# Optimization experiments

Hardware: AMD Instinct MI355X
Metric: run time of the kernel (lower is better)

## Reference

```python
import jax, jax.numpy as jnp
import numpy as np

N_NODES = 100000
N_EDGES = 1600000
N_GRAPHS = 256
F_NODE, F_EDGE, HID, OUT = 64, 16, 128, 128
BN_SCALE = 1.0 / np.sqrt(1.0 + 1e-5)  # BatchNorm eval with running mean 0, var 1


def setup_inputs() -> dict:
    key = jax.random.key(0)
    ks = iter(jax.random.split(key, 64))
    inp = {}
    inp["x"] = jax.random.normal(next(ks), (N_NODES, F_NODE), dtype=jnp.float32)
    inp["edge_attr"] = jax.random.normal(next(ks), (N_EDGES, F_EDGE), dtype=jnp.float32)
    inp["edge_index"] = jax.random.randint(next(ks), (2, N_EDGES), 0, N_NODES)
    inp["batch"] = jnp.sort(jax.random.randint(next(ks), (N_NODES,), 0, N_GRAPHS))

    def p(shape, scale):
        return (jax.random.normal(next(ks), shape, dtype=jnp.float32) * scale)

    in_dims = [F_NODE, HID, HID]
    for i, d in enumerate(in_dims):
        inp[f"el_w{i}"] = p((F_EDGE, d), F_EDGE ** -0.5)
        inp[f"el_b{i}"] = jnp.zeros((d,), jnp.float32)
        inp[f"c{i}_w1"] = p((d, HID), d ** -0.5)
        inp[f"c{i}_b1"] = jnp.zeros((HID,), jnp.float32)
        inp[f"c{i}_g"] = jnp.ones((HID,), jnp.float32)
        inp[f"c{i}_bt"] = jnp.zeros((HID,), jnp.float32)
        inp[f"c{i}_w2"] = p((HID, HID), HID ** -0.5)
        inp[f"c{i}_b2"] = jnp.zeros((HID,), jnp.float32)
    inp["o_w1"] = p((HID, OUT), HID ** -0.5)
    inp["o_b1"] = jnp.zeros((OUT,), jnp.float32)
    inp["o_w2"] = p((OUT, OUT), OUT ** -0.5)
    inp["o_b2"] = jnp.zeros((OUT,), jnp.float32)
    return inp


def reference(x, edge_attr,
              el_w0, el_b0, c0_w1, c0_b1, c0_g, c0_bt, c0_w2, c0_b2,
              el_w1, el_b1, c1_w1, c1_b1, c1_g, c1_bt, c1_w2, c1_b2,
              el_w2, el_b2, c2_w1, c2_b1, c2_g, c2_bt, c2_w2, c2_b2,
              o_w1, o_b1, o_w2, o_b2,
              edge_index, batch):
    src, dst = edge_index[0], edge_index[1]
    n = x.shape[0]
    layers = [
        (el_w0, el_b0, c0_w1, c0_b1, c0_g, c0_bt, c0_w2, c0_b2),
        (el_w1, el_b1, c1_w1, c1_b1, c1_g, c1_bt, c1_w2, c1_b2),
        (el_w2, el_b2, c2_w1, c2_b1, c2_g, c2_bt, c2_w2, c2_b2),
    ]
    h = x
    for (ew, eb, w1, b1, g, bt, w2, b2) in layers:
        ea = edge_attr @ ew + eb                              # [E, d]
        msg = jax.nn.relu(h[src] + ea)                        # GINEConv message
        agg = jax.ops.segment_sum(msg, dst, num_segments=n)   # scatter-sum to targets
        hh = h + agg                                          # (1+eps)*x + aggr, eps=0
        hh = hh @ w1 + b1                                     # MLP: Linear
        hh = g * (hh * BN_SCALE) + bt                         # BatchNorm1d (eval)
        hh = jax.nn.relu(hh)
        hh = hh @ w2 + b2                                     # MLP: Linear
        h = jax.nn.relu(hh)                                   # dropout(p=0, eval) + act
    s = jax.ops.segment_sum(h, batch, num_segments=N_GRAPHS)
    cnt = jax.ops.segment_sum(jnp.ones((n,), h.dtype), batch, num_segments=N_GRAPHS)
    pooled = s / jnp.maximum(cnt, 1.0)[:, None]               # scatter-mean pooling
    out = jax.nn.relu(pooled @ o_w1 + o_b1) @ o_w2 + o_b2     # out_lin
    return out
```

## Files before the change

kernel.cpp:

```cpp
#include <hip/hip_runtime.h>
#include <hip/hip_fp16.h>
#include <cstdint>
#include <cstddef>

#define N_NODES_C  100000
#define N_EDGES_C  1600000
#define N_GRAPHS_C 256
#define HID_C      128
#define BN_SCALE_C 0.9999950000374997f

#define SCAN_B 1024
#define SCAN_NB ((N_NODES_C + SCAN_B - 1) / SCAN_B)

struct __align__(16) H8 { __half2 v[4]; };

__global__ __launch_bounds__(256) void hist_kernel(
    const int* __restrict__ dst, int* __restrict__ counts, int n_edges)
{
    int e = blockIdx.x * 256 + threadIdx.x;
    if (e < n_edges) atomicAdd(&counts[dst[e]], 1);
}

__global__ __launch_bounds__(SCAN_B) void scan1_kernel(
    const int* __restrict__ counts, int* __restrict__ incl,
    int* __restrict__ blocksums, int n)
{
    __shared__ int sdata[SCAN_B];
    const int lid = threadIdx.x;
    const int i = blockIdx.x * SCAN_B + lid;
    sdata[lid] = (i < n) ? counts[i] : 0;
    __syncthreads();
#pragma unroll
    for (int off = 1; off < SCAN_B; off <<= 1) {
        int t = (lid >= off) ? sdata[lid - off] : 0;
        __syncthreads();
        sdata[lid] += t;
        __syncthreads();
    }
    if (i < n) incl[i] = sdata[lid];
    if (lid == SCAN_B - 1) blocksums[blockIdx.x] = sdata[lid];
}

__global__ void scan2_kernel(const int* __restrict__ blocksums,
                             int* __restrict__ blockoffs, int nb)
{
    if (threadIdx.x == 0 && blockIdx.x == 0) {
        int off = 0;
        for (int b = 0; b < nb; ++b) { blockoffs[b] = off; off += blocksums[b]; }
    }
}

__global__ __launch_bounds__(SCAN_B) void scan3_kernel(
    int* __restrict__ incl, const int* __restrict__ blockoffs, int n)
{
    const int i = blockIdx.x * SCAN_B + threadIdx.x;
    if (i < n) incl[i] += blockoffs[blockIdx.x];
}

__global__ __launch_bounds__(256) void initrows_kernel(
    const int* __restrict__ incl, const int* __restrict__ counts,
    int* __restrict__ rowstart, int* __restrict__ cursor, int n)
{
    const int i = blockIdx.x * 256 + threadIdx.x;
    if (i < n) {
        const int rs = incl[i] - counts[i];
        rowstart[i] = rs;
        cursor[i]   = rs;
    }
}

__global__ __launch_bounds__(256) void scatter_kernel(
    const int* __restrict__ src, const int* __restrict__ dst,
    int* __restrict__ cursor, int* __restrict__ perm_src,
    int* __restrict__ perm_eid, int n_edges)
{
    const int e = blockIdx.x * 256 + threadIdx.x;
    if (e < n_edges) {
        const int pos = atomicAdd(&cursor[dst[e]], 1);
        perm_src[pos] = src[e];
        perm_eid[pos] = e;
    }
}

__global__ __launch_bounds__(256) void permute_ea_f16_kernel(
    const float* __restrict__ edge_attr, const int* __restrict__ perm_eid,
    __half* __restrict__ ea_f16, int n_edges)
{
    const int j = blockIdx.x * 256 + threadIdx.x;
    if (j >= n_edges) return;
    const int eid = perm_eid[j];
    const float4* p = (const float4*)(edge_attr + (size_t)eid * 16);
    const float4 q0 = p[0], q1 = p[1], q2 = p[2], q3 = p[3];
    H8 a, b;
    a.v[0] = __floats2half2_rn(q0.x, q0.y);
    a.v[1] = __floats2half2_rn(q0.z, q0.w);
    a.v[2] = __floats2half2_rn(q1.x, q1.y);
    a.v[3] = __floats2half2_rn(q1.z, q1.w);
    b.v[0] = __floats2half2_rn(q2.x, q2.y);
    b.v[1] = __floats2half2_rn(q2.z, q2.w);
    b.v[2] = __floats2half2_rn(q3.x, q3.y);
    b.v[3] = __floats2half2_rn(q3.z, q3.w);
    H8* o = (H8*)(ea_f16 + (size_t)j * 16);
    o[0] = a;
    o[1] = b;
}

__device__ __forceinline__ float4 eamlp_f16(const H8* __restrict__ p,
                                            const __half2 (*ew2)[4],
                                            const float4 ebv)
{
    const H8 a = p[0], b = p[1];
    __half2 c0 = {0.f, 0.f}, c1 = {0.f, 0.f}, c2 = {0.f, 0.f}, c3 = {0.f, 0.f};
#pragma unroll
    for (int k2 = 0; k2 < 4; ++k2) {
        c0 = __hfma2(a.v[k2], ew2[k2][0], c0);
        c1 = __hfma2(a.v[k2], ew2[k2][1], c1);
        c2 = __hfma2(a.v[k2], ew2[k2][2], c2);
        c3 = __hfma2(a.v[k2], ew2[k2][3], c3);
    }
#pragma unroll
    for (int k2 = 0; k2 < 4; ++k2) {
        c0 = __hfma2(b.v[k2], ew2[4 + k2][0], c0);
        c1 = __hfma2(b.v[k2], ew2[4 + k2][1], c1);
        c2 = __hfma2(b.v[k2], ew2[4 + k2][2], c2);
        c3 = __hfma2(b.v[k2], ew2[4 + k2][3], c3);
    }
    float4 m;
    m.x = ebv.x + __low2float(c0) + __high2float(c0);
    m.y = ebv.y + __low2float(c1) + __high2float(c1);
    m.z = ebv.z + __low2float(c2) + __high2float(c2);
    m.w = ebv.w + __low2float(c3) + __high2float(c3);
    return m;
}

template<int DIN>
__global__ __launch_bounds__(256) void gine_agg_kernel(
    const float* __restrict__ h, const __half* __restrict__ ea_f16,
    const int* __restrict__ perm_src,
    const int* __restrict__ rowstart, const int* __restrict__ rowend,
    const float* __restrict__ ew, const float* __restrict__ eb,
    float* __restrict__ agg, int n_nodes)
{
    constexpr int NQ    = DIN / 4;
    constexpr int SLOTS = 256 / NQ;
    const int fq   = threadIdx.x & (NQ - 1);
    const int slot = threadIdx.x / NQ;
    const int v = blockIdx.x * SLOTS + slot;
    if (v >= n_nodes) return;

    __half2 ew2[8][4];
#pragma unroll
    for (int k2 = 0; k2 < 8; ++k2)
#pragma unroll
        for (int fi = 0; fi < 4; ++fi)
            ew2[k2][fi] = __floats2half2_rn(ew[(size_t)(2 * k2)     * DIN + fq * 4 + fi],
                                            ew[(size_t)(2 * k2 + 1) * DIN + fq * 4 + fi]);
    const float4 ebv = *(const float4*)(eb + fq * 4);

    const int s0 = rowstart[v];
    const int s1 = rowend[v];

    float4 acc = {0.f, 0.f, 0.f, 0.f};
    int j = s0;
    for (; j + 2 <= s1; j += 2) {
        const int sn0 = perm_src[j + 0];
        const int sn1 = perm_src[j + 1];
        const float4 hv0 = *(const float4*)(h + (size_t)sn0 * DIN + fq * 4);
        const float4 hv1 = *(const float4*)(h + (size_t)sn1 * DIN + fq * 4);
        const H8* p0 = (const H8*)(ea_f16 + (size_t)(j + 0) * 16);
        const H8* p1 = (const H8*)(ea_f16 + (size_t)(j + 1) * 16);
        const float4 m0 = eamlp_f16(p0, ew2, ebv);
        const float4 m1 = eamlp_f16(p1, ew2, ebv);
        acc.x += fmaxf(m0.x + hv0.x, 0.f) + fmaxf(m1.x + hv1.x, 0.f);
        acc.y += fmaxf(m0.y + hv0.y, 0.f) + fmaxf(m1.y + hv1.y, 0.f);
        acc.z += fmaxf(m0.z + hv0.z, 0.f) + fmaxf(m1.z + hv1.z, 0.f);
        acc.w += fmaxf(m0.w + hv0.w, 0.f) + fmaxf(m1.w + hv1.w, 0.f);
    }
    if (j < s1) {
        const int sn = perm_src[j];
        const float4 hv = *(const float4*)(h + (size_t)sn * DIN + fq * 4);
        const H8* p = (const H8*)(ea_f16 + (size_t)j * 16);
        const float4 m = eamlp_f16(p, ew2, ebv);
        acc.x += fmaxf(m.x + hv.x, 0.f);
        acc.y += fmaxf(m.y + hv.y, 0.f);
        acc.z += fmaxf(m.z + hv.z, 0.f);
        acc.w += fmaxf(m.w + hv.w, 0.f);
    }
    *(float4*)(agg + (size_t)v * DIN + fq * 4) = acc;
}

#define OUT4(acc, a0, a1, a2, a3, wv)                                     \
    do {                                                                  \
        acc[0][0] = fmaf(a0, wv.x, acc[0][0]);                            \
        acc[0][1] = fmaf(a0, wv.y, acc[0][1]);                            \
        acc[0][2] = fmaf(a0, wv.z, acc[0][2]);                            \
        acc[0][3] = fmaf(a0, wv.w, acc[0][3]);                            \
        acc[1][0] = fmaf(a1, wv.x, acc[1][0]);                            \
        acc[1][1] = fmaf(a1, wv.y, acc[1][1]);                            \
        acc[1][2] = fmaf(a1, wv.z, acc[1][2]);                            \
        acc[1][3] = fmaf(a1, wv.w, acc[1][3]);                            \
        acc[2][0] = fmaf(a2, wv.x, acc[2][0]);                            \
        acc[2][1] = fmaf(a2, wv.y, acc[2][1]);                            \
        acc[2][2] = fmaf(a2, wv.z, acc[2][2]);                            \
        acc[2][3] = fmaf(a2, wv.w, acc[2][3]);                            \
        acc[3][0] = fmaf(a3, wv.x, acc[3][0]);                            \
        acc[3][1] = fmaf(a3, wv.y, acc[3][1]);                            \
        acc[3][2] = fmaf(a3, wv.z, acc[3][2]);                            \
        acc[3][3] = fmaf(a3, wv.w, acc[3][3]);                            \
    } while (0)

template<int DIN>
__global__ __launch_bounds__(256) void node_kernel(
    const float* __restrict__ h, const float* __restrict__ agg,
    const float* __restrict__ w1, const float* __restrict__ b1,
    const float* __restrict__ gm, const float* __restrict__ bt,
    const float* __restrict__ w2, const float* __restrict__ b2,
    float* __restrict__ hout, int n_nodes)
{
    constexpr int SX = DIN + 4;
    constexpr int ST = HID_C + 4;
    __shared__ float s_x[32][SX];
    __shared__ float s_t[32][ST];

    const int tid = threadIdx.x;
    const int fg = tid & 31;
    const int ng = tid >> 5;
    const int base = blockIdx.x * 32;

    constexpr int KQ = DIN / 4;
    for (int idx = tid; idx < 32 * KQ; idx += 256) {
        const int ni = idx / KQ;
        const int k4 = (idx - ni * KQ) * 4;
        const int node = base + ni;
        const float4 hv = *(const float4*)(h   + (size_t)node * DIN + k4);
        const float4 av = *(const float4*)(agg + (size_t)node * DIN + k4);
        float4 s; s.x = hv.x + av.x; s.y = hv.y + av.y;
        s.z = hv.z + av.z; s.w = hv.w + av.w;
        *(float4*)(&s_x[ni][k4]) = s;
    }
    __syncthreads();

    {
        const float4 b1v = *(const float4*)(b1 + fg * 4);
        float acc[4][4];
#pragma unroll
        for (int ni = 0; ni < 4; ++ni) {
            acc[ni][0] = b1v.x; acc[ni][1] = b1v.y;
            acc[ni][2] = b1v.z; acc[ni][3] = b1v.w;
        }
        for (int k = 0; k < DIN; k += 4) {
            const float4 x0 = *(const float4*)(&s_x[ng * 4 + 0][k]);
            const float4 x1 = *(const float4*)(&s_x[ng * 4 + 1][k]);
            const float4 x2 = *(const float4*)(&s_x[ng * 4 + 2][k]);
            const float4 x3 = *(const float4*)(&s_x[ng * 4 + 3][k]);
            const float4 wa = *(const float4*)(w1 + (size_t)(k + 0) * HID_C + fg * 4);
            const float4 wb = *(const float4*)(w1 + (size_t)(k + 1) * HID_C + fg * 4);
            const float4 wc = *(const float4*)(w1 + (size_t)(k + 2) * HID_C + fg * 4);
            const float4 wd = *(const float4*)(w1 + (size_t)(k + 3) * HID_C + fg * 4);
            OUT4(acc, x0.x, x1.x, x2.x, x3.x, wa);
            OUT4(acc, x0.y, x1.y, x2.y, x3.y, wb);
            OUT4(acc, x0.z, x1.z, x2.z, x3.z, wc);
            OUT4(acc, x0.w, x1.w, x2.w, x3.w, wd);
        }
        const float4 gv  = *(const float4*)(gm + fg * 4);
        const float4 btv = *(const float4*)(bt + fg * 4);
#pragma unroll
        for (int ni = 0; ni < 4; ++ni) {
            float4 tv;
            tv.x = fmaxf(fmaf(acc[ni][0] * BN_SCALE_C, gv.x, btv.x), 0.f);
            tv.y = fmaxf(fmaf(acc[ni][1] * BN_SCALE_C, gv.y, btv.y), 0.f);
            tv.z = fmaxf(fmaf(acc[ni][2] * BN_SCALE_C, gv.z, btv.z), 0.f);
            tv.w = fmaxf(fmaf(acc[ni][3] * BN_SCALE_C, gv.w, btv.w), 0.f);
            *(float4*)(&s_t[ng * 4 + ni][fg * 4]) = tv;
        }
    }
    __syncthreads();

    {
        const float4 b2v = *(const float4*)(b2 + fg * 4);
        float acc[4][4];
#pragma unroll
        for (int ni = 0; ni < 4; ++ni) {
            acc[ni][0] = b2v.x; acc[ni][1] = b2v.y;
            acc[ni][2] = b2v.z; acc[ni][3] = b2v.w;
        }
        for (int k = 0; k < HID_C; k += 4) {
            const float4 x0 = *(const float4*)(&s_t[ng * 4 + 0][k]);
            const float4 x1 = *(const float4*)(&s_t[ng * 4 + 1][k]);
            const float4 x2 = *(const float4*)(&s_t[ng * 4 + 2][k]);
            const float4 x3 = *(const float4*)(&s_t[ng * 4 + 3][k]);
            const float4 wa = *(const float4*)(w2 + (size_t)(k + 0) * HID_C + fg * 4);
            const float4 wb = *(const float4*)(w2 + (size_t)(k + 1) * HID_C + fg * 4);
            const float4 wc = *(const float4*)(w2 + (size_t)(k + 2) * HID_C + fg * 4);
            const float4 wd = *(const float4*)(w2 + (size_t)(k + 3) * HID_C + fg * 4);
            OUT4(acc, x0.x, x1.x, x2.x, x3.x, wa);
            OUT4(acc, x0.y, x1.y, x2.y, x3.y, wb);
            OUT4(acc, x0.z, x1.z, x2.z, x3.z, wc);
            OUT4(acc, x0.w, x1.w, x2.w, x3.w, wd);
        }
#pragma unroll
        for (int ni = 0; ni < 4; ++ni) {
            const int node = base + ng * 4 + ni;
            float4 ov;
            ov.x = fmaxf(acc[ni][0], 0.f);
            ov.y = fmaxf(acc[ni][1], 0.f);
            ov.z = fmaxf(acc[ni][2], 0.f);
            ov.w = fmaxf(acc[ni][3], 0.f);
            *(float4*)(hout + (size_t)node * HID_C + fg * 4) = ov;
        }
    }
}

__global__ __launch_bounds__(256) void pool_kernel(
    const float* __restrict__ hfin, const int* __restrict__ batch,
    const float* __restrict__ w1, const float* __restrict__ b1,
    const float* __restrict__ w2, const float* __restrict__ b2,
    float* __restrict__ out, int n_nodes)
{
    const int gid = blockIdx.x;

    int lo = 0, hi = n_nodes;
    while (lo < hi) { int mid = (lo + hi) >> 1; if (batch[mid] < gid) lo = mid + 1; else hi = mid; }
    const int start = lo;
    hi = n_nodes;
    while (lo < hi) { int mid = (lo + hi) >> 1; if (batch[mid] < gid + 1) lo = mid + 1; else hi = mid; }
    const int end = lo;

    const int f = threadIdx.x & (HID_C - 1);
    const int half = threadIdx.x >> 7;

    float sum = 0.f;
    for (int n = start + half; n < end; n += 2)
        sum += hfin[(size_t)n * HID_C + f];

    __shared__ float s_sum[2][HID_C];
    __shared__ float s_p[HID_C];
    __shared__ float s_t[HID_C];
    s_sum[half][f] = sum;
    __syncthreads();

    if (threadIdx.x < HID_C) {
        const float cnt = (float)(end - start);
        s_p[f] = (s_sum[0][f] + s_sum[1][f]) / fmaxf(cnt, 1.f);
    }
    __syncthreads();

    if (threadIdx.x < HID_C) {
        float acc = b1[f];
        for (int k = 0; k < HID_C; ++k) acc = fmaf(s_p[k], w1[k * HID_C + f], acc);
        s_t[f] = fmaxf(acc, 0.f);
    }
    __syncthreads();

    if (threadIdx.x < HID_C) {
        float acc = b2[f];
        for (int k = 0; k < HID_C; ++k) acc = fmaf(s_t[k], w2[k * HID_C + f], acc);
        out[(size_t)gid * HID_C + f] = acc;
    }
}

extern "C" void kernel_launch(void* const* d_in, const int* in_sizes, int n_in,
                              void* d_out, int out_size, void* d_ws, size_t ws_size,
                              hipStream_t stream)
{
    const float* x         = (const float*)d_in[0];
    const float* edge_attr = (const float*)d_in[1];
    const int*   edge_index= (const int*)  d_in[2];
    const int*   batch     = (const int*)  d_in[3];
    const int*   src = edge_index;
    const int*   dst = edge_index + N_EDGES_C;

    const float* el_w[3] = {(const float*)d_in[4],  (const float*)d_in[12], (const float*)d_in[20]};
    const float* el_b[3] = {(const float*)d_in[5],  (const float*)d_in[13], (const float*)d_in[21]};
    const float* c_w1[3] = {(const float*)d_in[6],  (const float*)d_in[14], (const float*)d_in[22]};
    const float* c_b1[3] = {(const float*)d_in[7],  (const float*)d_in[15], (const float*)d_in[23]};
    const float* c_g [3] = {(const float*)d_in[8],  (const float*)d_in[16], (const float*)d_in[24]};
    const float* c_bt[3] = {(const float*)d_in[9],  (const float*)d_in[17], (const float*)d_in[25]};
    const float* c_w2[3] = {(const float*)d_in[10], (const float*)d_in[18], (const float*)d_in[26]};
    const float* c_b2[3] = {(const float*)d_in[11], (const float*)d_in[19], (const float*)d_in[27]};
    const float* o_w1 = (const float*)d_in[28];
    const float* o_b1 = (const float*)d_in[29];
    const float* o_w2 = (const float*)d_in[30];
    const float* o_b2 = (const float*)d_in[31];

    char* wsp = (char*)d_ws;
    size_t used = 0;
    auto alloc = [&](size_t bytes) { char* p = wsp + used; used += (bytes + 255) & ~(size_t)255; return p; };
    float* h        = (float*)alloc((size_t)N_NODES_C * HID_C * 4);
    float* agg      = (float*)alloc((size_t)N_NODES_C * HID_C * 4);
    int*   counts   = (int*)alloc((size_t)N_NODES_C * 4);
    int*   incl     = (int*)alloc((size_t)N_NODES_C * 4);
    int*   rowstart = (int*)alloc((size_t)N_NODES_C * 4);
    int*   cursor   = (int*)alloc((size_t)N_NODES_C * 4);
    int*   blocksums= (int*)alloc(128 * 4);
    int*   blockoffs= (int*)alloc(128 * 4);
    int*   perm_src = (int*)alloc((size_t)N_EDGES_C * 4);
    int*   perm_eid = (int*)alloc((size_t)N_EDGES_C * 4);
    __half* ea_f16  = (__half*)alloc((size_t)N_EDGES_C * 16 * 2);
    (void)ws_size;

    hipMemsetAsync(counts, 0, (size_t)N_NODES_C * 4, stream);
    hist_kernel<<<(N_EDGES_C + 255) / 256, 256, 0, stream>>>(dst, counts, N_EDGES_C);
    scan1_kernel<<<SCAN_NB, SCAN_B, 0, stream>>>(counts, incl, blocksums, N_NODES_C);
    scan2_kernel<<<1, 64, 0, stream>>>(blocksums, blockoffs, SCAN_NB);
    scan3_kernel<<<SCAN_NB, SCAN_B, 0, stream>>>(incl, blockoffs, N_NODES_C);
    initrows_kernel<<<(N_NODES_C + 255) / 256, 256, 0, stream>>>(incl, counts, rowstart,
                                                                 cursor, N_NODES_C);
    scatter_kernel<<<(N_EDGES_C + 255) / 256, 256, 0, stream>>>(src, dst, cursor,
                                                                perm_src, perm_eid, N_EDGES_C);
    permute_ea_f16_kernel<<<(N_EDGES_C + 255) / 256, 256, 0, stream>>>(
        edge_attr, perm_eid, ea_f16, N_EDGES_C);

    for (int l = 0; l < 3; ++l) {
        const float* hin = (l == 0) ? x : h;
        if (l == 0) {
            gine_agg_kernel<64><<<(N_NODES_C + 15) / 16, 256, 0, stream>>>(
                hin, ea_f16, perm_src, rowstart, incl, el_w[0], el_b[0],
                agg, N_NODES_C);
            node_kernel<64><<<N_NODES_C / 32, 256, 0, stream>>>(
                hin, agg, c_w1[0], c_b1[0], c_g[0], c_bt[0], c_w2[0], c_b2[0],
                h, N_NODES_C);
        } else {
            gine_agg_kernel<128><<<(N_NODES_C + 7) / 8, 256, 0, stream>>>(
                hin, ea_f16, perm_src, rowstart, incl, el_w[l], el_b[l],
                agg, N_NODES_C);
            node_kernel<128><<<N_NODES_C / 32, 256, 0, stream>>>(
                hin, agg, c_w1[l], c_b1[l], c_g[l], c_bt[l], c_w2[l], c_b2[l],
                h, N_NODES_C);
        }
    }

    pool_kernel<<<N_GRAPHS_C, 256, 0, stream>>>(h, batch, o_w1, o_b1, o_w2, o_b2,
                                                (float*)d_out, N_NODES_C);
}
```

Measured before the change: 1.163 ms.

## Gather fp16 node features in aggregation and run node MLP on MFMA

The edge aggregation now gathers source-node features from an fp16 copy of h (and of x for layer 0), which halves the bytes moved by the random gather. The node MLP is rewritten as a per-wave 16-node tile using mfma_f32_16x16x32_f16, with the weights pre-transposed to fp16 by small setup kernels. The node kernel also emits the fp16 copy of h for the next layer. The cost is extra fp16 rounding of activations and weights, plus a few setup kernels and extra writes.

```diff
diff --git a/kernel.cpp b/kernel.cpp
--- a/kernel.cpp
+++ b/kernel.cpp
@@ -12,7 +12,12 @@
 #define SCAN_B 1024
 #define SCAN_NB ((N_NODES_C + SCAN_B - 1) / SCAN_B)
 
+typedef _Float16 h8 __attribute__((ext_vector_type(8)));
+typedef _Float16 h4 __attribute__((ext_vector_type(4)));
+typedef float    f4 __attribute__((ext_vector_type(4)));
+
 struct __align__(16) H8 { __half2 v[4]; };
+struct __align__(8)  Hq { __half2 a, b; };
 
 __global__ __launch_bounds__(256) void hist_kernel(
     const int* __restrict__ dst, int* __restrict__ counts, int n_edges)
@@ -105,6 +110,27 @@
     o[1] = b;
 }
 
+__global__ __launch_bounds__(256) void cast_f16_kernel(
+    const float* __restrict__ in, _Float16* __restrict__ out, int n4)
+{
+    const int i = blockIdx.x * 256 + threadIdx.x;
+    if (i >= n4) return;
+    const float4 v = ((const float4*)in)[i];
+    h4 o; o[0] = (_Float16)v.x; o[1] = (_Float16)v.y;
+    o[2] = (_Float16)v.z; o[3] = (_Float16)v.w;
+    *(h4*)(out + (size_t)i * 4) = o;
+}
+
+__global__ __launch_bounds__(256) void transpose_w_kernel(
+    const float* __restrict__ w, _Float16* __restrict__ wt, int K, int N)
+{
+    const int i = blockIdx.x * 256 + threadIdx.x;
+    if (i >= K * N) return;
+    const int n = i / K;
+    const int k = i - n * K;
+    wt[(size_t)n * K + k] = (_Float16)w[(size_t)k * N + n];
+}
+
 __device__ __forceinline__ float4 eamlp_f16(const H8* __restrict__ p,
                                             const __half2 (*ew2)[4],
                                             const float4 ebv)
@@ -135,7 +161,7 @@
 
 template<int DIN>
 __global__ __launch_bounds__(256) void gine_agg_kernel(
-    const float* __restrict__ h, const __half* __restrict__ ea_f16,
+    const __half* __restrict__ h16, const __half* __restrict__ ea_f16,
     const int* __restrict__ perm_src,
     const int* __restrict__ rowstart, const int* __restrict__ rowend,
     const float* __restrict__ ew, const float* __restrict__ eb,
@@ -165,148 +191,107 @@
     for (; j + 2 <= s1; j += 2) {
         const int sn0 = perm_src[j + 0];
         const int sn1 = perm_src[j + 1];
-        const float4 hv0 = *(const float4*)(h + (size_t)sn0 * DIN + fq * 4);
-        const float4 hv1 = *(const float4*)(h + (size_t)sn1 * DIN + fq * 4);
+        const Hq hq0 = *(const Hq*)(h16 + (size_t)sn0 * DIN + fq * 4);
+        const Hq hq1 = *(const Hq*)(h16 + (size_t)sn1 * DIN + fq * 4);
         const H8* p0 = (const H8*)(ea_f16 + (size_t)(j + 0) * 16);
         const H8* p1 = (const H8*)(ea_f16 + (size_t)(j + 1) * 16);
         const float4 m0 = eamlp_f16(p0, ew2, ebv);
         const float4 m1 = eamlp_f16(p1, ew2, ebv);
-        acc.x += fmaxf(m0.x + hv0.x, 0.f) + fmaxf(m1.x + hv1.x, 0.f);
-        acc.y += fmaxf(m0.y + hv0.y, 0.f) + fmaxf(m1.y + hv1.y, 0.f);
-        acc.z += fmaxf(m0.z + hv0.z, 0.f) + fmaxf(m1.z + hv1.z, 0.f);
-        acc.w += fmaxf(m0.w + hv0.w, 0.f) + fmaxf(m1.w + hv1.w, 0.f);
+        const float2 l0 = __half22float2(hq0.a), u0 = __half22float2(hq0.b);
+        const float2 l1 = __half22float2(hq1.a), u1 = __half22float2(hq1.b);
+        acc.x += fmaxf(m0.x + l0.x, 0.f) + fmaxf(m1.x + l1.x, 0.f);
+        acc.y += fmaxf(m0.y + l0.y, 0.f) + fmaxf(m1.y + l1.y, 0.f);
+        acc.z += fmaxf(m0.z + u0.x, 0.f) + fmaxf(m1.z + u1.x, 0.f);
+        acc.w += fmaxf(m0.w + u0.y, 0.f) + fmaxf(m1.w + u1.y, 0.f);
     }
     if (j < s1) {
         const int sn = perm_src[j];
-        const float4 hv = *(const float4*)(h + (size_t)sn * DIN + fq * 4);
+        const Hq hq = *(const Hq*)(h16 + (size_t)sn * DIN + fq * 4);
         const H8* p = (const H8*)(ea_f16 + (size_t)j * 16);
         const float4 m = eamlp_f16(p, ew2, ebv);
-        acc.x += fmaxf(m.x + hv.x, 0.f);
-        acc.y += fmaxf(m.y + hv.y, 0.f);
-        acc.z += fmaxf(m.z + hv.z, 0.f);
-        acc.w += fmaxf(m.w + hv.w, 0.f);
+        const float2 l = __half22float2(hq.a), u = __half22float2(hq.b);
+        acc.x += fmaxf(m.x + l.x, 0.f);
+        acc.y += fmaxf(m.y + l.y, 0.f);
+        acc.z += fmaxf(m.z + u.x, 0.f);
+        acc.w += fmaxf(m.w + u.y, 0.f);
     }
     *(float4*)(agg + (size_t)v * DIN + fq * 4) = acc;
 }
 
-#define OUT4(acc, a0, a1, a2, a3, wv)                                     \
-    do {                                                                  \
-        acc[0][0] = fmaf(a0, wv.x, acc[0][0]);                            \
-        acc[0][1] = fmaf(a0, wv.y, acc[0][1]);                            \
-        acc[0][2] = fmaf(a0, wv.z, acc[0][2]);                            \
-        acc[0][3] = fmaf(a0, wv.w, acc[0][3]);                            \
-        acc[1][0] = fmaf(a1, wv.x, acc[1][0]);                            \
-        acc[1][1] = fmaf(a1, wv.y, acc[1][1]);                            \
-        acc[1][2] = fmaf(a1, wv.z, acc[1][2]);                            \
-        acc[1][3] = fmaf(a1, wv.w, acc[1][3]);                            \
-        acc[2][0] = fmaf(a2, wv.x, acc[2][0]);                            \
-        acc[2][1] = fmaf(a2, wv.y, acc[2][1]);                            \
-        acc[2][2] = fmaf(a2, wv.z, acc[2][2]);                            \
-        acc[2][3] = fmaf(a2, wv.w, acc[2][3]);                            \
-        acc[3][0] = fmaf(a3, wv.x, acc[3][0]);                            \
-        acc[3][1] = fmaf(a3, wv.y, acc[3][1]);                            \
-        acc[3][2] = fmaf(a3, wv.z, acc[3][2]);                            \
-        acc[3][3] = fmaf(a3, wv.w, acc[3][3]);                            \
-    } while (0)
-
 template<int DIN>
-__global__ __launch_bounds__(256) void node_kernel(
+__global__ __launch_bounds__(256) void node_mfma_kernel(
     const float* __restrict__ h, const float* __restrict__ agg,
-    const float* __restrict__ w1, const float* __restrict__ b1,
+    const _Float16* __restrict__ w1t, const float* __restrict__ b1,
     const float* __restrict__ gm, const float* __restrict__ bt,
-    const float* __restrict__ w2, const float* __restrict__ b2,
-    float* __restrict__ hout, int n_nodes)
-{
-    constexpr int SX = DIN + 4;
-    constexpr int ST = HID_C + 4;
-    __shared__ float s_x[32][SX];
-    __shared__ float s_t[32][ST];
-
-    const int tid = threadIdx.x;
-    const int fg = tid & 31;
-    const int ng = tid >> 5;
-    const int base = blockIdx.x * 32;
+    const _Float16* __restrict__ w2t, const float* __restrict__ b2,
+    float* __restrict__ hout, _Float16* __restrict__ h16out, int n_tiles)
+{
+    constexpr int SXP = DIN + 8;
+    constexpr int STP = HID_C + 8;
+    __shared__ _Float16 s_x[4][16][SXP];
+    __shared__ _Float16 s_t[4][16][STP];
+
+    const int w    = threadIdx.x >> 6;
+    const int lane = threadIdx.x & 63;
+    int tile = blockIdx.x * 4 + w;
+    if (tile >= n_tiles) tile = n_tiles - 1;
+    const int node0 = tile * 16;
 
     constexpr int KQ = DIN / 4;
-    for (int idx = tid; idx < 32 * KQ; idx += 256) {
-        const int ni = idx / KQ;
-        const int k4 = (idx - ni * KQ) * 4;
-        const int node = base + ni;
-        const float4 hv = *(const float4*)(h   + (size_t)node * DIN + k4);
-        const float4 av = *(const float4*)(agg + (size_t)node * DIN + k4);
-        float4 s; s.x = hv.x + av.x; s.y = hv.y + av.y;
-        s.z = hv.z + av.z; s.w = hv.w + av.w;
-        *(float4*)(&s_x[ni][k4]) = s;
-    }
-    __syncthreads();
-
-    {
-        const float4 b1v = *(const float4*)(b1 + fg * 4);
-        float acc[4][4];
-#pragma unroll
-        for (int ni = 0; ni < 4; ++ni) {
-            acc[ni][0] = b1v.x; acc[ni][1] = b1v.y;
-            acc[ni][2] = b1v.z; acc[ni][3] = b1v.w;
+    for (int it = lane; it < 16 * KQ; it += 64) {
+        const int ni = it / KQ;
+        const int k4 = (it - ni * KQ) * 4;
+        const float4 hv = *(const float4*)(h   + (size_t)(node0 + ni) * DIN + k4);
+        const float4 av = *(const float4*)(agg + (size_t)(node0 + ni) * DIN + k4);
+        h4 o;
+        o[0] = (_Float16)(hv.x + av.x);
+        o[1] = (_Float16)(hv.y + av.y);
+        o[2] = (_Float16)(hv.z + av.z);
+        o[3] = (_Float16)(hv.w + av.w);
+        *(h4*)&s_x[w][ni][k4] = o;
+    }
+    __syncthreads();
+
+    const int ln   = lane & 15;
+    const int quad = lane >> 4;
+
+#pragma unroll
+    for (int nt = 0; nt < 8; ++nt) {
+        const int col = nt * 16 + ln;
+        const float bv = b1[col];
+        f4 acc = {bv, bv, bv, bv};
+#pragma unroll
+        for (int ks = 0; ks < DIN / 32; ++ks) {
+            const h8 af = *(const h8*)&s_x[w][ln][ks * 32 + quad * 8];
+            const h8 bf = *(const h8*)(w1t + (size_t)col * DIN + ks * 32 + quad * 8);
+            acc = __builtin_amdgcn_mfma_f32_16x16x32_f16(af, bf, acc, 0, 0, 0);
         }
-        for (int k = 0; k < DIN; k += 4) {
-            const float4 x0 = *(const float4*)(&s_x[ng * 4 + 0][k]);
-            const float4 x1 = *(const float4*)(&s_x[ng * 4 + 1][k]);
-            const float4 x2 = *(const float4*)(&s_x[ng * 4 + 2][k]);
-            const float4 x3 = *(const float4*)(&s_x[ng * 4 + 3][k]);
-            const float4 wa = *(const float4*)(w1 + (size_t)(k + 0) * HID_C + fg * 4);
-            const float4 wb = *(const float4*)(w1 + (size_t)(k + 1) * HID_C + fg * 4);
-            const float4 wc = *(const float4*)(w1 + (size_t)(k + 2) * HID_C + fg * 4);
-            const float4 wd = *(const float4*)(w1 + (size_t)(k + 3) * HID_C + fg * 4);
-            OUT4(acc, x0.x, x1.x, x2.x, x3.x, wa);
-            OUT4(acc, x0.y, x1.y, x2.y, x3.y, wb);
-            OUT4(acc, x0.z, x1.z, x2.z, x3.z, wc);
-            OUT4(acc, x0.w, x1.w, x2.w, x3.w, wd);
+        const float gv = gm[col], btv = bt[col];
+#pragma unroll
+        for (int r = 0; r < 4; ++r) {
+            const float t = fmaxf(fmaf(acc[r] * BN_SCALE_C, gv, btv), 0.f);
+            s_t[w][quad * 4 + r][col] = (_Float16)t;
         }
-        const float4 gv  = *(const float4*)(gm + fg * 4);
-        const float4 btv = *(const float4*)(bt + fg * 4);
-#pragma unroll
-        for (int ni = 0; ni < 4; ++ni) {
-            float4 tv;
-            tv.x = fmaxf(fmaf(acc[ni][0] * BN_SCALE_C, gv.x, btv.x), 0.f);
-            tv.y = fmaxf(fmaf(acc[ni][1] * BN_SCALE_C, gv.y, btv.y), 0.f);
-            tv.z = fmaxf(fmaf(acc[ni][2] * BN_SCALE_C, gv.z, btv.z), 0.f);
-            tv.w = fmaxf(fmaf(acc[ni][3] * BN_SCALE_C, gv.w, btv.w), 0.f);
-            *(float4*)(&s_t[ng * 4 + ni][fg * 4]) = tv;
+    }
+    __syncthreads();
+
+#pragma unroll
+    for (int nt = 0; nt < 8; ++nt) {
+        const int col = nt * 16 + ln;
+        const float bv = b2[col];
+        f4 acc = {bv, bv, bv, bv};
+#pragma unroll
+        for (int ks = 0; ks < HID_C / 32; ++ks) {
+            const h8 af = *(const h8*)&s_t[w][ln][ks * 32 + quad * 8];
+            const h8 bf = *(const h8*)(w2t + (size_t)col * HID_C + ks * 32 + quad * 8);
+            acc = __builtin_amdgcn_mfma_f32_16x16x32_f16(af, bf, acc, 0, 0, 0);
         }
-    }
-    __syncthreads();
-
-    {
-        const float4 b2v = *(const float4*)(b2 + fg * 4);
-        float acc[4][4];
-#pragma unroll
-        for (int ni = 0; ni < 4; ++ni) {
-            acc[ni][0] = b2v.x; acc[ni][1] = b2v.y;
-            acc[ni][2] = b2v.z; acc[ni][3] = b2v.w;
-        }
-        for (int k = 0; k < HID_C; k += 4) {
-            const float4 x0 = *(const float4*)(&s_t[ng * 4 + 0][k]);
-            const float4 x1 = *(const float4*)(&s_t[ng * 4 + 1][k]);
-            const float4 x2 = *(const float4*)(&s_t[ng * 4 + 2][k]);
-            const float4 x3 = *(const float4*)(&s_t[ng * 4 + 3][k]);
-            const float4 wa = *(const float4*)(w2 + (size_t)(k + 0) * HID_C + fg * 4);
-            const float4 wb = *(const float4*)(w2 + (size_t)(k + 1) * HID_C + fg * 4);
-            const float4 wc = *(const float4*)(w2 + (size_t)(k + 2) * HID_C + fg * 4);
-            const float4 wd = *(const float4*)(w2 + (size_t)(k + 3) * HID_C + fg * 4);
-            OUT4(acc, x0.x, x1.x, x2.x, x3.x, wa);
-            OUT4(acc, x0.y, x1.y, x2.y, x3.y, wb);
-            OUT4(acc, x0.z, x1.z, x2.z, x3.z, wc);
-            OUT4(acc, x0.w, x1.w, x2.w, x3.w, wd);
-        }
-#pragma unroll
-        for (int ni = 0; ni < 4; ++ni) {
-            const int node = base + ng * 4 + ni;
-            float4 ov;
-            ov.x = fmaxf(acc[ni][0], 0.f);
-            ov.y = fmaxf(acc[ni][1], 0.f);
-            ov.z = fmaxf(acc[ni][2], 0.f);
-            ov.w = fmaxf(acc[ni][3], 0.f);
-            *(float4*)(hout + (size_t)node * HID_C + fg * 4) = ov;
+#pragma unroll
+        for (int r = 0; r < 4; ++r) {
+            const int node = node0 + quad * 4 + r;
+            const float v = fmaxf(acc[r], 0.f);
+            hout[(size_t)node * HID_C + col] = v;
+            h16out[(size_t)node * HID_C + col] = (_Float16)v;
         }
     }
 }
@@ -396,7 +381,14 @@
     int*   blockoffs= (int*)alloc(128 * 4);
     int*   perm_src = (int*)alloc((size_t)N_EDGES_C * 4);
     int*   perm_eid = (int*)alloc((size_t)N_EDGES_C * 4);
-    __half* ea_f16  = (__half*)alloc((size_t)N_EDGES_C * 16 * 2);
+    __half*    ea_f16 = (__half*)alloc((size_t)N_EDGES_C * 16 * 2);
+    _Float16*  h_f16  = (_Float16*)alloc((size_t)N_NODES_C * HID_C * 2);
+    _Float16*  x_f16  = (_Float16*)alloc((size_t)N_NODES_C * 64 * 2);
+    _Float16*  w1t[3], *w2t[3];
+    for (int l = 0; l < 3; ++l) {
+        w1t[l] = (_Float16*)alloc((size_t)HID_C * HID_C * 2);
+        w2t[l] = (_Float16*)alloc((size_t)HID_C * HID_C * 2);
+    }
     (void)ws_size;
 
     hipMemsetAsync(counts, 0, (size_t)N_NODES_C * 4, stream);
@@ -410,23 +402,34 @@
                                                                 perm_src, perm_eid, N_EDGES_C);
     permute_ea_f16_kernel<<<(N_EDGES_C + 255) / 256, 256, 0, stream>>>(
         edge_attr, perm_eid, ea_f16, N_EDGES_C);
-
+    cast_f16_kernel<<<(N_NODES_C * 64 / 4 + 255) / 256, 256, 0, stream>>>(
+        x, x_f16, N_NODES_C * 64 / 4);
     for (int l = 0; l < 3; ++l) {
-        const float* hin = (l == 0) ? x : h;
+        const int K1 = (l == 0) ? 64 : HID_C;
+        transpose_w_kernel<<<(K1 * HID_C + 255) / 256, 256, 0, stream>>>(
+            c_w1[l], w1t[l], K1, HID_C);
+        transpose_w_kernel<<<(HID_C * HID_C + 255) / 256, 256, 0, stream>>>(
+            c_w2[l], w2t[l], HID_C, HID_C);
+    }
+
+    const int n_tiles = N_NODES_C / 16;
+    const int nb_node = (n_tiles + 3) / 4;
+
+    for (int l = 0; l < 3; ++l) {
         if (l == 0) {
             gine_agg_kernel<64><<<(N_NODES_C + 15) / 16, 256, 0, stream>>>(
-                hin, ea_f16, perm_src, rowstart, incl, el_w[0], el_b[0],
-                agg, N_NODES_C);
-            node_kernel<64><<<N_NODES_C / 32, 256, 0, stream>>>(
-                hin, agg, c_w1[0], c_b1[0], c_g[0], c_bt[0], c_w2[0], c_b2[0],
-                h, N_NODES_C);
+                (const __half*)x_f16, ea_f16, perm_src, rowstart, incl,
+                el_w[0], el_b[0], agg, N_NODES_C);
+            node_mfma_kernel<64><<<nb_node, 256, 0, stream>>>(
+                x, agg, w1t[0], c_b1[0], c_g[0], c_bt[0], w2t[0], c_b2[0],
+                h, h_f16, n_tiles);
         } else {
             gine_agg_kernel<128><<<(N_NODES_C + 7) / 8, 256, 0, stream>>>(
-                hin, ea_f16, perm_src, rowstart, incl, el_w[l], el_b[l],
-                agg, N_NODES_C);
-            node_kernel<128><<<N_NODES_C / 32, 256, 0, stream>>>(
-                hin, agg, c_w1[l], c_b1[l], c_g[l], c_bt[l], c_w2[l], c_b2[l],
-                h, N_NODES_C);
+                (const __half*)h_f16, ea_f16, perm_src, rowstart, incl,
+                el_w[l], el_b[l], agg, N_NODES_C);
+            node_mfma_kernel<128><<<nb_node, 256, 0, stream>>>(
+                h, agg, w1t[l], c_b1[l], c_g[l], c_bt[l], w2t[l], c_b2[l],
+                h, h_f16, n_tiles);
         }
     }
 
```

Measured after the change: 1.104 ms. 1.05x faster.
